# Kernel tuning notes

Hardware: AMD Instinct MI355X
Metric: run time of the kernel (lower is better)

The kernel has to match this reference:

```python
import jax, jax.numpy as jnp
import numpy as np

B, L, D, H, K = 4, 2048, 256, 8, 32
DH = D // H
DE = 64          # d_edge
CLIP = 32        # relpos_clip


def _ln(x, g, b):
    mu = x.mean(-1, keepdims=True)
    var = ((x - mu) ** 2).mean(-1, keepdims=True)
    return (x - mu) / jnp.sqrt(var + 1e-5) * g + b


def _gelu(x):
    return jax.nn.gelu(x, approximate=False)  # torch nn.GELU default = exact erf


def _masked_softmax(logits, mask):
    logits = jnp.where(mask == 0, jnp.finfo(logits.dtype).min, logits)
    return jax.nn.softmax(logits, axis=-1)


def setup_inputs() -> dict:
    key = jax.random.key(0)
    ks = jax.random.split(key, 24)
    s = 0.02
    w = lambda i, shape: jax.random.normal(ks[i], shape, jnp.float32) * s
    p = {}
    p['x'] = jax.random.normal(ks[0], (B, L, D), jnp.float32)
    p['mask'] = jax.random.randint(ks[1], (B, L), 0, 2, jnp.int32)
    p['nbr_idx'] = jax.random.randint(ks[2], (B, L, K), 0, L, jnp.int32)
    p['nbr_mask'] = jax.random.randint(ks[3], (B, L, K), 0, 2, jnp.int32)
    p['rel_pos'] = jax.random.randint(ks[4], (B, L, K), 0, 2 * CLIP + 1, jnp.int32)
    p['g1'] = jnp.ones((D,)); p['b1'] = jnp.zeros((D,))
    p['wq'] = w(5, (D, D)); p['wk'] = w(6, (D, D)); p['wv'] = w(7, (D, D))
    p['relpos_emb'] = w(8, (2 * CLIP + 1, DE))
    p['we1'] = w(9, (DE, D)); p['be1'] = jnp.zeros((D,))
    p['we2'] = w(10, (D, 1)); p['be2'] = jnp.zeros((1,))
    p['wg1'] = w(11, (2 * D, D)); p['bg1'] = jnp.zeros((D,))
    p['wg2'] = w(12, (D, D)); p['bg2'] = jnp.zeros((D,))
    p['wlo'] = w(13, (D, D)); p['blo'] = jnp.zeros((D,))
    p['wqkv'] = w(14, (D, 3 * D)); p['wgo'] = w(15, (D, D))
    p['wf1'] = w(16, (D, D)); p['bf1'] = jnp.zeros((D,))
    p['wf2'] = w(17, (D, 2)); p['bf2'] = jnp.zeros((2,))
    p['g2'] = jnp.ones((D,)); p['b2'] = jnp.zeros((D,))
    p['wff1'] = w(18, (D, 4 * D)); p['bff1'] = jnp.zeros((4 * D,))
    p['wff2'] = w(19, (4 * D, D)); p['bff2'] = jnp.zeros((D,))
    return p


def _block(x, mask, nbr_idx, nbr_mask, rel_pos,
           g1, b1, wq, wk, wv, relpos_emb, we1, be1, we2, be2,
           wg1, bg1, wg2, bg2, wlo, blo, wqkv, wgo,
           wf1, bf1, wf2, bf2, g2, b2, wff1, bff1, wff2, bff2):
    mf = mask.astype(x.dtype)                       # [B,L]
    h = _ln(x, g1, b1)

    # ---- local graph attention (gather over K neighbors) ----
    neigh = jax.vmap(lambda hb, ib: hb[ib])(h, nbr_idx)     # [B,L,K,D]
    q = (h @ wq)[:, :, None, :]                             # [B,L,1,D]
    k = neigh @ wk                                          # [B,L,K,D]
    v = neigh @ wv
    attn = (q * k).sum(-1) / np.sqrt(D).astype(np.float32)  # [B,L,K]
    rel = jnp.clip(rel_pos, -CLIP, CLIP) + CLIP
    e = relpos_emb[rel]                                     # [B,L,K,DE]
    attn = attn + (_gelu(e @ we1 + be1) @ we2 + be2)[..., 0]
    amask = nbr_mask * mask[:, :, None]
    w = _masked_softmax(attn, amask)
    agg = jnp.einsum('blk,blkd->bld', w, v)
    agg = agg @ wlo + blo
    g = jax.nn.sigmoid(_gelu(jnp.concatenate([h, agg], -1) @ wg1 + bg1) @ wg2 + bg2)
    h_local = (h + g * agg) * mf[..., None]

    # ---- global linear attention ----
    qkv = h @ wqkv
    qg, kg, vg = jnp.split(qkv, 3, axis=-1)
    to_heads = lambda z: z.reshape(B, L, H, DH).transpose(0, 2, 1, 3)  # [B,H,L,DH]
    qg, kg, vg = to_heads(qg), to_heads(kg), to_heads(vg)
    phi = lambda z: jax.nn.elu(z) + 1.0
    qg, kg = phi(qg), phi(kg)
    m = mf[:, None, :, None]
    kg = kg * m
    vg = vg * m
    kv = jnp.einsum('bhld,bhlm->bhdm', kg, vg)
    z = 1.0 / (jnp.einsum('bhld,bhd->bhl', qg, kg.sum(axis=2)) + 1e-6)
    y = jnp.einsum('bhld,bhdm->bhlm', qg, kv) * z[..., None]
    y = y.transpose(0, 2, 1, 3).reshape(B, L, D)
    y = (y @ wgo) * mf[..., None]
    h_global = h + y

    # ---- gated fusion (softmax over 2 branches) ----
    fw = jax.nn.softmax(_gelu(h @ wf1 + bf1) @ wf2 + bf2, axis=-1)
    yc = fw[..., 0:1] * h_local + fw[..., 1:2] * h_global
    x2 = x + (yc - x)  # DropPath is identity in eval mode

    # ---- FFN ----
    hn = _ln(x2, g2, b2)
    ffn = _gelu(hn @ wff1 + bff1) @ wff2 + bff2
    out = (x2 + ffn) * mf[..., None]
    return out


def reference(x, mask, nbr_idx, nbr_mask, rel_pos,
              g1, b1, wq, wk, wv, relpos_emb, we1, be1, we2, be2,
              wg1, bg1, wg2, bg2, wlo, blo, wqkv, wgo,
              wf1, bf1, wf2, bf2, g2, b2, wff1, bff1, wff2, bff2):
    return _block(x, mask, nbr_idx, nbr_mask, rel_pos,
                  g1, b1, wq, wk, wv, relpos_emb, we1, be1, we2, be2,
                  wg1, bg1, wg2, bg2, wlo, blo, wqkv, wgo,
                  wf1, bf1, wf2, bf2, g2, b2, wff1, bff1, wff2, bff2)
```

## Files before the change

kernel.cpp:

```cpp
#include <hip/hip_runtime.h>
#include <math.h>

#define LSEQ 2048
#define BB 4
#define DD 256
#define NROWS (BB*LSEQ)
#define LDBIG 1792

typedef unsigned short u16;
typedef unsigned int u32;
typedef short s16x8 __attribute__((ext_vector_type(8)));
typedef float f32x4 __attribute__((ext_vector_type(4)));

#define WT_BIG  0
#define WT_LO   458752
#define WT_G1   524288
#define WT_G2   655360
#define WT_GO   720896
#define WT_FF1  786432
#define WT_FF2  1048576
#define WT_TMP1 1310720
#define WT_TMP2 1376256

__device__ __forceinline__ float gelu_f(float x){
    return 0.5f*x*(1.0f+erff(x*0.70710678118654752440f));
}
__device__ __forceinline__ float phi_f(float z){ return z>0.f ? z+1.f : expf(z); }
__device__ __forceinline__ float bf2f(u16 u){ union{u32 i; float f;} x; x.i = ((u32)u)<<16; return x.f; }
__device__ __forceinline__ u16 f2bf(float f){ union{float f; u32 i;} x; x.f = f; u32 r = (x.i + 0x7fff + ((x.i>>16)&1)) >> 16; return (u16)r; }

struct TransDesc { const float* src; int dstoff; int srcK; int N; int dstStride; int tstart; };
struct TransArgs { TransDesc d[12]; };

__global__ __launch_bounds__(256) void prep_kernel(
    TransArgs args, u16* __restrict__ WT,
    const float* __restrict__ x, const float* __restrict__ g1,
    const float* __restrict__ b1, u16* __restrict__ h,
    const float* __restrict__ emb, const float* __restrict__ we1,
    const float* __restrict__ be1, const float* __restrict__ we2,
    const float* __restrict__ be2, float* __restrict__ btab,
    float* __restrict__ kvz,
    const float* __restrict__ wlo, const float* __restrict__ wg1,
    const float* __restrict__ blo, const float* __restrict__ bg1,
    float* __restrict__ bprime)
{
    int bid = blockIdx.x;
    if (bid < 1280){
        int z = 0;
        #pragma unroll
        for (int i=1;i<12;++i) if (bid >= args.d[i].tstart) z = i;
        TransDesc e = args.d[z];
        int tid = bid - e.tstart;
        int ntx = e.N >> 5;
        int kt = tid / ntx, nt = tid - kt*ntx;
        __shared__ float tile[32][33];
        int tx = threadIdx.x & 31, ty = threadIdx.x >> 5;
        #pragma unroll
        for (int i=0;i<4;++i){
            int k = kt*32 + ty + i*8;
            tile[ty+i*8][tx] = e.src[(size_t)k*e.N + nt*32 + tx];
        }
        __syncthreads();
        #pragma unroll
        for (int i=0;i<4;++i){
            int n = nt*32 + ty + i*8;
            WT[e.dstoff + (size_t)n*e.dstStride + kt*32 + tx] = f2bf(tile[tx][ty+i*8]);
        }
    } else if (bid < 9472){
        int r = bid - 1280; int t = threadIdx.x;
        size_t i = (size_t)r*DD + t;
        float v = x[i];
        float s = v, ss = v*v;
        #pragma unroll
        for (int o=32;o>=1;o>>=1){ s += __shfl_xor(s,o); ss += __shfl_xor(ss,o); }
        __shared__ float sh[8];
        int wave = t>>6, lane = t&63;
        if (lane==0){ sh[wave]=s; sh[4+wave]=ss; }
        __syncthreads();
        float S  = sh[0]+sh[1]+sh[2]+sh[3];
        float SS = sh[4]+sh[5]+sh[6]+sh[7];
        float mu  = S*(1.f/DD);
        float var = SS*(1.f/DD) - mu*mu;
        float inv = rsqrtf(var + 1e-5f);
        h[i] = f2bf((v-mu)*inv*g1[t] + b1[t]);
    } else if (bid < 9537){
        int r = bid - 9472; int j = threadIdx.x;
        float acc = be1[j];
        #pragma unroll 8
        for (int d=0; d<64; ++d) acc += emb[r*64+d]*we1[d*256+j];
        float tv = gelu_f(acc)*we2[j];
        #pragma unroll
        for (int o=32;o>=1;o>>=1) tv += __shfl_xor(tv,o);
        __shared__ float sh2[4];
        int wave = j>>6, lane = j&63;
        if (lane==0) sh2[wave]=tv;
        __syncthreads();
        if (j==0) btab[r] = sh2[0]+sh2[1]+sh2[2]+sh2[3] + be2[0];
    } else if (bid < 9669){
        int idx = (bid - 9537)*256 + threadIdx.x;
        kvz[idx] = 0.f;
    } else if (bid < 9733){
        int idx = (bid - 9669)*1024 + threadIdx.x*4;
        float4 v = *(const float4*)&wlo[idx];
        u32 lo = (u32)f2bf(v.x) | ((u32)f2bf(v.y)<<16);
        u32 hi = (u32)f2bf(v.z) | ((u32)f2bf(v.w)<<16);
        *(u32*)&WT[WT_TMP2 + idx]     = lo;
        *(u32*)&WT[WT_TMP2 + idx + 2] = hi;
    } else {
        int t = threadIdx.x;
        float a = bg1[t];
        for (int m=0;m<256;++m) a += blo[m]*wg1[(size_t)(256+m)*256 + t];
        bprime[t] = a;
    }
}

template<int ACT, bool FINAL, typename CT>
__device__ __forceinline__ void mgemm_core(
    const u16* __restrict__ A0, const u16* __restrict__ A1, int kswitch, int lda,
    const u16* __restrict__ WT, int Kd,
    const float* __restrict__ bias, int actcol,
    CT* __restrict__ C, int ldc,
    const u16* __restrict__ addsrc, const int* __restrict__ rowmask,
    int row0, int col0)
{
    __shared__ u16 ldsA[4096];
    __shared__ u16 ldsB[8192];
    int t = threadIdx.x;
    int l = t & 63, w = t >> 6;
    int wm = w >> 1, wn = w & 1;

    int s_ar = t >> 2, s_ao = t & 3;
    int aidx1 = (s_ar>>4)*1024 + s_ao*128 + (s_ar&15)*8;
    int aidx2 = aidx1 + 4*128;
    int s_bc = t >> 1, s_bo = (t & 1)*4;
    int bbase = (s_bc>>4)*1024 + (s_bc&15)*8;

    f32x4 acc[2][4];
    #pragma unroll
    for (int mf=0;mf<2;++mf)
        #pragma unroll
        for (int nf=0;nf<4;++nf)
            acc[mf][nf] = (f32x4){0.f,0.f,0.f,0.f};

    uint4 av1, av2, bv0, bv1, bv2, bv3;
    {
        const u16* ap = A0 + (size_t)(row0+s_ar)*lda;
        av1 = *(const uint4*)(ap + s_ao*8);
        av2 = *(const uint4*)(ap + 32 + s_ao*8);
        const u16* bp = WT + (size_t)(col0 + s_bc)*Kd + s_bo*8;
        bv0 = *(const uint4*)(bp); bv1 = *(const uint4*)(bp+8);
        bv2 = *(const uint4*)(bp+16); bv3 = *(const uint4*)(bp+24);
    }

    for (int k0 = 0; k0 < Kd; k0 += 64){
        __syncthreads();
        *(uint4*)&ldsA[aidx1] = av1;
        *(uint4*)&ldsA[aidx2] = av2;
        *(uint4*)&ldsB[bbase + (s_bo  )*128] = bv0;
        *(uint4*)&ldsB[bbase + (s_bo+1)*128] = bv1;
        *(uint4*)&ldsB[bbase + (s_bo+2)*128] = bv2;
        *(uint4*)&ldsB[bbase + (s_bo+3)*128] = bv3;
        __syncthreads();
        int kn = k0 + 64;
        if (kn < Kd){
            const u16* Ab = A0; int kk = kn;
            if (kn >= kswitch){ Ab = A1; kk = kn - kswitch; }
            const u16* ap = Ab + (size_t)(row0+s_ar)*lda + kk;
            av1 = *(const uint4*)(ap + s_ao*8);
            av2 = *(const uint4*)(ap + 32 + s_ao*8);
            const u16* bp = WT + (size_t)(col0 + s_bc)*Kd + kn + s_bo*8;
            bv0 = *(const uint4*)(bp); bv1 = *(const uint4*)(bp+8);
            bv2 = *(const uint4*)(bp+16); bv3 = *(const uint4*)(bp+24);
        }
        #pragma unroll
        for (int s=0;s<2;++s){
            s16x8 af[2], bfr[4];
            #pragma unroll
            for (int mf=0;mf<2;++mf) af[mf] = *(s16x8*)&ldsA[(wm*2+mf)*1024 + (s*4+(l>>4))*128 + (l&15)*8];
            #pragma unroll
            for (int nf=0;nf<4;++nf) bfr[nf] = *(s16x8*)&ldsB[(wn*4+nf)*1024 + (s*4+(l>>4))*128 + (l&15)*8];
            #pragma unroll
            for (int mf=0; mf<2; ++mf)
                #pragma unroll
                for (int nf=0; nf<4; ++nf)
                    acc[mf][nf] = __builtin_amdgcn_mfma_f32_16x16x32_bf16(af[mf], bfr[nf], acc[mf][nf], 0,0,0);
        }
    }

    int lrow = (l>>4)*4, lcol = l&15;
    #pragma unroll
    for (int mf=0; mf<2; ++mf){
        #pragma unroll
        for (int nf=0; nf<4; ++nf){
            int col = col0 + wn*64 + nf*16 + lcol;
            float bv;
            if (ACT==1) bv = (col >= actcol) ? bias[col-actcol] : 0.f;
            else        bv = bias ? bias[col] : 0.f;
            #pragma unroll
            for (int i=0;i<4;++i){
                int row = row0 + wm*32 + mf*16 + lrow + i;
                float v = acc[mf][nf][i] + bv;
                if (ACT==1){ if (col >= actcol) v = gelu_f(v); }
                else if (ACT==2) v = 1.f/(1.f+expf(-v));
                if (FINAL){
                    float mfv = (float)rowmask[row];
                    v = (bf2f(addsrc[(size_t)row*ldc + col]) + v) * mfv;
                }
                if constexpr (sizeof(CT)==2) C[(size_t)row*ldc+col] = (CT)f2bf(v);
                else                         C[(size_t)row*ldc+col] = v;
            }
        }
    }
}

template<int ACT, bool FINAL, typename CT>
__global__ __launch_bounds__(256) void mgemm(
    const u16* __restrict__ A0, const u16* __restrict__ A1, int kswitch, int lda,
    const u16* __restrict__ WT, int Kd,
    const float* __restrict__ bias, int actcol,
    CT* __restrict__ C, int ldc,
    const u16* __restrict__ addsrc, const int* __restrict__ rowmask)
{
    mgemm_core<ACT,FINAL,CT>(A0,A1,kswitch,lda,WT,Kd,bias,actcol,C,ldc,addsrc,rowmask,
                             blockIdx.x*64, blockIdx.y*128);
}

struct GemmCfg { const u16* A0; const u16* A1; int kswitch; const u16* WT; int Kd;
                 const float* bias; int act; u16* C; };
__global__ __launch_bounds__(256) void mgemm_tri(GemmCfg c0, GemmCfg c1, GemmCfg c2)
{
    GemmCfg c = (blockIdx.z==0) ? c0 : ((blockIdx.z==1) ? c1 : c2);
    if (c.act==1)
        mgemm_core<1,false,u16>(c.A0, c.A1, c.kswitch, 256, c.WT, c.Kd, c.bias, 0,
                                c.C, 256, nullptr, nullptr, blockIdx.x*64, blockIdx.y*128);
    else
        mgemm_core<0,false,u16>(c.A0, c.A1, c.kswitch, 256, c.WT, c.Kd, c.bias, 0,
                                c.C, 256, nullptr, nullptr, blockIdx.x*64, blockIdx.y*128);
}

__global__ __launch_bounds__(256) void nattn_kernel(
    const u16* __restrict__ nb,
    const int* __restrict__ nbr_idx, const int* __restrict__ nbr_mask,
    const int* __restrict__ rel_pos, const int* __restrict__ mask,
    const float* __restrict__ btab, u16* __restrict__ agg)
{
    int r = blockIdx.x;
    int b = r >> 11;
    int t = threadIdx.x, lane = t&63, wave = t>>6;
    __shared__ float s_w[32];
    __shared__ float s_agg[4][256];
    uint2 qu = *(const uint2*)&nb[(size_t)r*LDBIG + lane*4];
    float q0 = bf2f(qu.x&0xffff), q1 = bf2f(qu.x>>16);
    float q2 = bf2f(qu.y&0xffff), q3 = bf2f(qu.y>>16);
    int mrow = mask[r];

    uint2 kreg[8], vreg[8];
    #pragma unroll
    for (int j=0;j<8;++j){
        int idx = nbr_idx[r*32 + wave*8 + j];
        size_t grow = ((size_t)(b<<11) + idx)*LDBIG;
        kreg[j] = *(const uint2*)&nb[grow + 256 + lane*4];
        vreg[j] = *(const uint2*)&nb[grow + 512 + lane*4];
    }
    float d[8];
    #pragma unroll
    for (int j=0;j<8;++j){
        d[j] = q0*bf2f(kreg[j].x&0xffff) + q1*bf2f(kreg[j].x>>16)
             + q2*bf2f(kreg[j].y&0xffff) + q3*bf2f(kreg[j].y>>16);
    }
    #define CMB(a,b,s) ({ float _t = (lane&(s)) ? (a) : (b); float _r = __shfl_xor(_t,(s)); (lane&(s)) ? ((b)+_r) : ((a)+_r); })
    float e10 = CMB(d[0],d[1],1), e11 = CMB(d[2],d[3],1);
    float e12 = CMB(d[4],d[5],1), e13 = CMB(d[6],d[7],1);
    float e20 = CMB(e10,e11,2),   e21 = CMB(e12,e13,2);
    float e3  = CMB(e20,e21,4);
    #undef CMB
    e3 += __shfl_xor(e3,8); e3 += __shfl_xor(e3,16); e3 += __shfl_xor(e3,32);
    if (lane < 8){
        int k = wave*8 + lane;
        int rp = rel_pos[r*32+k];
        rp = rp < -32 ? -32 : (rp > 32 ? 32 : rp);
        float logit = e3*0.0625f + btab[rp+32];
        int am = nbr_mask[r*32+k] * mrow;
        s_w[k] = am ? logit : -3.402823466e38f;
    }
    __syncthreads();
    if (wave==0){
        float lg = (lane<32) ? s_w[lane] : -3.402823466e38f;
        float m = lg;
        #pragma unroll
        for (int o=16;o>=1;o>>=1) m = fmaxf(m, __shfl_xor(m,o));
        float e = (lane<32) ? expf(lg-m) : 0.f;
        float ssum = e;
        #pragma unroll
        for (int o=16;o>=1;o>>=1) ssum += __shfl_xor(ssum,o);
        if (lane<32) s_w[lane] = e/ssum;
    }
    __syncthreads();
    float4 av = {0.f,0.f,0.f,0.f};
    #pragma unroll
    for (int j=0;j<8;++j){
        float wk = s_w[wave*8 + j];
        av.x += wk*bf2f(vreg[j].x&0xffff); av.y += wk*bf2f(vreg[j].x>>16);
        av.z += wk*bf2f(vreg[j].y&0xffff); av.w += wk*bf2f(vreg[j].y>>16);
    }
    *(float4*)&s_agg[wave][lane*4] = av;
    __syncthreads();
    float sum = s_agg[0][t]+s_agg[1][t]+s_agg[2][t]+s_agg[3][t];
    agg[(size_t)r*256 + t] = f2bf(sum);
}

__global__ __launch_bounds__(256) void linstats_kernel(
    const u16* __restrict__ qkv, const int* __restrict__ mask,
    float* __restrict__ kv, float* __restrict__ ksum)
{
    int blk = blockIdx.x;
    int bh = blk >> 4, ch = blk & 15;
    int b = bh >> 3, hh = bh & 7;
    int t = threadIdx.x;
    int d = t >> 3, m4 = (t & 7)*4;
    __shared__ float sk[8][32], sv[8][32];
    float a0=0,a1=0,a2=0,a3=0, aks=0;
    int l0 = ch*128;
    int half = t >> 7, tt = t & 127;
    int lr = tt >> 4, e2 = (tt & 15)*2;
    for (int g8=0; g8<16; ++g8){
        int l = l0 + g8*8 + lr;
        size_t base = ((size_t)b*LSEQ + l)*LDBIG + (half ? 1280 : 1024) + hh*32 + e2;
        u32 u = *(const u32*)&qkv[base];
        float mf = (float)mask[b*LSEQ + l];
        float x0 = bf2f((u16)(u & 0xffff));
        float x1 = bf2f((u16)(u >> 16));
        if (half==0){ sk[lr][e2] = phi_f(x0)*mf; sk[lr][e2+1] = phi_f(x1)*mf; }
        else        { sv[lr][e2] = x0*mf;        sv[lr][e2+1] = x1*mf; }
        __syncthreads();
        #pragma unroll
        for (int rr=0;rr<8;++rr){
            float kd = sk[rr][d];
            a0 += kd*sv[rr][m4]; a1 += kd*sv[rr][m4+1];
            a2 += kd*sv[rr][m4+2]; a3 += kd*sv[rr][m4+3];
            if ((t&7)==0) aks += kd;
        }
        __syncthreads();
    }
    size_t kb = (size_t)bh*1024 + d*32 + m4;
    atomicAdd(&kv[kb+0],a0); atomicAdd(&kv[kb+1],a1);
    atomicAdd(&kv[kb+2],a2); atomicAdd(&kv[kb+3],a3);
    if ((t&7)==0) atomicAdd(&ksum[bh*32+d], aks);
}

__global__ __launch_bounds__(256) void linapply_kernel(
    const u16* __restrict__ qkv, const float* __restrict__ kv,
    const float* __restrict__ ksum, u16* __restrict__ y)
{
    int r = blockIdx.x; int b = r >> 11;
    int t = threadIdx.x;
    __shared__ float sq[256];
    if (t < 128){
        u32 u = *(const u32*)&qkv[(size_t)r*LDBIG + 768 + t*2];
        sq[t*2]   = phi_f(bf2f((u16)(u & 0xffff)));
        sq[t*2+1] = phi_f(bf2f((u16)(u >> 16)));
    }
    __syncthreads();
    int hh = t>>5, m = t&31;
    const float* kvb = &kv[(size_t)((b<<3)+hh)*1024 + m];
    const float* ksb = &ksum[((b<<3)+hh)*32];
    const float* sqh = &sq[hh*32];
    float acc=0.f, az=0.f;
    #pragma unroll
    for (int dd=0; dd<32; ++dd){
        float qd = sqh[dd];
        acc += qd * kvb[dd*32];
        az  += qd * ksb[dd];
    }
    y[(size_t)r*256 + t] = f2bf(acc / (az + 1e-6f));
}

__global__ __launch_bounds__(128) void combine_kernel(
    const u16* __restrict__ h, const u16* __restrict__ agglo,
    const u16* __restrict__ g, const u16* __restrict__ ygo,
    const u16* __restrict__ bigout, const float* __restrict__ wf2,
    const float* __restrict__ bf2v, const int* __restrict__ mask,
    const float* __restrict__ g2, const float* __restrict__ b2,
    u16* __restrict__ x2, u16* __restrict__ hn)
{
    int r = blockIdx.x, t = threadIdx.x;
    int wave = t>>6, lane = t&63;
    u32 fu = *(const u32*)&bigout[(size_t)r*LDBIG + 1536 + t*2];
    float fa = bf2f((u16)(fu&0xffff)), fb = bf2f((u16)(fu>>16));
    int dd = t*2;
    float p0 = fa*wf2[dd*2]   + fb*wf2[dd*2+2];
    float p1 = fa*wf2[dd*2+1] + fb*wf2[dd*2+3];
    #pragma unroll
    for (int o=32;o>=1;o>>=1){ p0 += __shfl_xor(p0,o); p1 += __shfl_xor(p1,o); }
    __shared__ float shp[4];
    if (lane==0){ shp[wave]=p0; shp[2+wave]=p1; }
    __syncthreads();
    float P0 = shp[0]+shp[1]+bf2v[0], P1 = shp[2]+shp[3]+bf2v[1];
    float mx = fmaxf(P0,P1);
    float e0 = expf(P0-mx), e1 = expf(P1-mx);
    float f0 = e0/(e0+e1), f1v = e1/(e0+e1);
    size_t i = (size_t)r*DD + t*2;
    float mf = (float)mask[r];
    u32 hu = *(const u32*)&h[i],  au = *(const u32*)&agglo[i];
    u32 gu = *(const u32*)&g[i],  yu = *(const u32*)&ygo[i];
    float hv0 = bf2f((u16)(hu&0xffff)), hv1 = bf2f((u16)(hu>>16));
    float ag0 = bf2f((u16)(au&0xffff)), ag1 = bf2f((u16)(au>>16));
    float gg0 = bf2f((u16)(gu&0xffff)), gg1 = bf2f((u16)(gu>>16));
    float yy0 = bf2f((u16)(yu&0xffff)), yy1 = bf2f((u16)(yu>>16));
    float v0 = f0*((hv0 + gg0*ag0)*mf) + f1v*(hv0 + yy0*mf);
    float v1 = f0*((hv1 + gg1*ag1)*mf) + f1v*(hv1 + yy1*mf);
    *(u32*)&x2[i] = (u32)f2bf(v0) | ((u32)f2bf(v1)<<16);
    float s = v0+v1, ss = v0*v0+v1*v1;
    #pragma unroll
    for (int o=32;o>=1;o>>=1){ s += __shfl_xor(s,o); ss += __shfl_xor(ss,o); }
    __shared__ float sh[4];
    if (lane==0){ sh[wave]=s; sh[2+wave]=ss; }
    __syncthreads();
    float S  = sh[0]+sh[1];
    float SS = sh[2]+sh[3];
    float mu  = S*(1.f/DD);
    float var = SS*(1.f/DD) - mu*mu;
    float inv = rsqrtf(var + 1e-5f);
    int j0 = t*2;
    float o0 = (v0-mu)*inv*g2[j0]   + b2[j0];
    float o1 = (v1-mu)*inv*g2[j0+1] + b2[j0+1];
    *(u32*)&hn[i] = (u32)f2bf(o0) | ((u32)f2bf(o1)<<16);
}

extern "C" void kernel_launch(void* const* d_in, const int* in_sizes, int n_in,
                              void* d_out, int out_size, void* d_ws, size_t ws_size,
                              hipStream_t stream)
{
    const float* x        = (const float*)d_in[0];
    const int*   mask     = (const int*)  d_in[1];
    const int*   nbr_idx  = (const int*)  d_in[2];
    const int*   nbr_mask = (const int*)  d_in[3];
    const int*   rel_pos  = (const int*)  d_in[4];
    const float* g1   = (const float*)d_in[5];
    const float* b1   = (const float*)d_in[6];
    const float* wq   = (const float*)d_in[7];
    const float* wk   = (const float*)d_in[8];
    const float* wv   = (const float*)d_in[9];
    const float* relpos_emb = (const float*)d_in[10];
    const float* we1  = (const float*)d_in[11];
    const float* be1  = (const float*)d_in[12];
    const float* we2  = (const float*)d_in[13];
    const float* be2  = (const float*)d_in[14];
    const float* wg1  = (const float*)d_in[15];
    const float* bg1  = (const float*)d_in[16];
    const float* wg2  = (const float*)d_in[17];
    const float* bg2  = (const float*)d_in[18];
    const float* wlo  = (const float*)d_in[19];
    const float* blo  = (const float*)d_in[20];
    const float* wqkv = (const float*)d_in[21];
    const float* wgo  = (const float*)d_in[22];
    const float* wf1  = (const float*)d_in[23];
    const float* bf1  = (const float*)d_in[24];
    const float* wf2  = (const float*)d_in[25];
    const float* bf2  = (const float*)d_in[26];
    const float* g2   = (const float*)d_in[27];
    const float* b2   = (const float*)d_in[28];
    const float* wff1 = (const float*)d_in[29];
    const float* bff1 = (const float*)d_in[30];
    const float* wff2 = (const float*)d_in[31];
    const float* bff2 = (const float*)d_in[32];
    float* out = (float*)d_out;

    unsigned char* wsb = (unsigned char*)d_ws;
    u16* bigout  = (u16*)(wsb + ((size_t)0<<20));
    u16* h_bf    = (u16*)(wsb + ((size_t)30<<20));
    u16* agg_bf  = (u16*)(wsb + ((size_t)34<<20));
    u16* agglo_bf= (u16*)(wsb + ((size_t)38<<20));
    u16* x2y_bf  = (u16*)(wsb + ((size_t)42<<20));
    u16* tg_bf   = (u16*)(wsb + ((size_t)46<<20));
    u16* ygo_bf  = (u16*)(wsb + ((size_t)50<<20));
    u16* hn_bf   = (u16*)(wsb + ((size_t)54<<20));
    u16* WT      = (u16*)(wsb + ((size_t)58<<20));
    float* btab  = (float*)(wsb + ((size_t)61<<20));
    float* kvb   = btab + 128;
    float* ksb   = kvb + 32768;
    float* bprime= ksb + 1024;

    TransArgs ta;
    ta.d[0]  = { wq,          WT_BIG + 0,       256,  256,  256,    0 };
    ta.d[1]  = { wk,          WT_BIG + 65536,   256,  256,  256,   64 };
    ta.d[2]  = { wv,          WT_BIG + 131072,  256,  256,  256,  128 };
    ta.d[3]  = { wqkv,        WT_BIG + 196608,  256,  768,  256,  192 };
    ta.d[4]  = { wf1,         WT_BIG + 393216,  256,  256,  256,  384 };
    ta.d[5]  = { wlo,         WT_LO,            256,  256,  256,  448 };
    ta.d[6]  = { wg1,         WT_G1,            256,  256,  512,  512 };
    ta.d[7]  = { wg2,         WT_G2,            256,  256,  256,  576 };
    ta.d[8]  = { wgo,         WT_GO,            256,  256,  256,  640 };
    ta.d[9]  = { wff1,        WT_FF1,           256, 1024,  256,  704 };
    ta.d[10] = { wff2,        WT_FF2,          1024,  256, 1024,  960 };
    ta.d[11] = { wg1+65536,   WT_TMP1,          256,  256,  256, 1216 };

    const int KBIG = 1<<30;
    dim3 blk(256);

    prep_kernel<<<9734, blk, 0, stream>>>(ta, WT, x, g1, b1, h_bf,
                                          relpos_emb, we1, be1, we2, be2, btab, kvb,
                                          wlo, wg1, blo, bg1, bprime);
    mgemm<0,false,u16><<<dim3(4,2), blk, 0, stream>>>(WT+WT_TMP1, WT+WT_TMP1, KBIG, 256,
                                                      WT+WT_TMP2, 256, nullptr, 0,
                                                      WT+WT_G1+256, 512, nullptr, nullptr);
    mgemm<1,false,u16><<<dim3(128,14), blk, 0, stream>>>(h_bf, h_bf, KBIG, 256, WT+WT_BIG, 256, bf1, 1536, bigout, LDBIG, nullptr, nullptr);
    linstats_kernel<<<512, blk, 0, stream>>>(bigout, mask, kvb, ksb);
    linapply_kernel<<<NROWS, blk, 0, stream>>>(bigout, kvb, ksb, x2y_bf);
    nattn_kernel<<<NROWS, blk, 0, stream>>>(bigout, nbr_idx, nbr_mask, rel_pos, mask, btab, agg_bf);
    {
        GemmCfg cgo = { x2y_bf, x2y_bf, KBIG, WT+WT_GO, 256, nullptr, 0, ygo_bf };
        GemmCfg clo = { agg_bf, agg_bf, KBIG, WT+WT_LO, 256, blo,     0, agglo_bf };
        GemmCfg cg1 = { h_bf,   agg_bf, 256,  WT+WT_G1, 512, bprime,  1, tg_bf };
        mgemm_tri<<<dim3(128,2,3), blk, 0, stream>>>(cgo, clo, cg1);
    }
    mgemm<2,false,u16><<<dim3(128,2), blk, 0, stream>>>(tg_bf, tg_bf, KBIG, 256, WT+WT_G2, 256, bg2, 0, agg_bf, 256, nullptr, nullptr);
    combine_kernel<<<NROWS, dim3(128), 0, stream>>>(h_bf, agglo_bf, agg_bf, ygo_bf, bigout, wf2, bf2, mask, g2, b2, x2y_bf, hn_bf);
    mgemm<1,false,u16><<<dim3(128,8), blk, 0, stream>>>(hn_bf, hn_bf, KBIG, 256, WT+WT_FF1, 256, bff1, 0, bigout, 1024, nullptr, nullptr);
    mgemm<0,true,float><<<dim3(128,2), blk, 0, stream>>>(bigout, bigout, KBIG, 1024, WT+WT_FF2, 1024, bff2, 0, out, 256, x2y_bf, mask);
}
```

Measured before the change: 285.2 us.

## Fuse gate GEMM with fusion/LayerNorm combine; shuffle-based softmax in neighbor attention

The separate wg2 GEMM (sigmoid gate) and the per-row combine kernel are merged into one kernel. Each block computes a 32-row by 256-column gate tile with MFMA, then applies the branch-softmax fusion, writes x2 and computes LayerNorm for hn in the same kernel. This removes one launch and the round-trip of the gate tensor through global memory. In exchange, only 256 blocks are launched, which may underuse the GPU, and the epilogue uses scattered 2-byte stores. The neighbor-attention softmax now runs redundantly in every wave with shuffles, replacing a wave-0-only pass plus an extra barrier.

After: 293.7 us. +3.0%, slower.

```diff
diff --git a/kernel.cpp b/kernel.cpp
--- a/kernel.cpp
+++ b/kernel.cpp
@@ -284,22 +284,19 @@
         s_w[k] = am ? logit : -3.402823466e38f;
     }
     __syncthreads();
-    if (wave==0){
-        float lg = (lane<32) ? s_w[lane] : -3.402823466e38f;
-        float m = lg;
-        #pragma unroll
-        for (int o=16;o>=1;o>>=1) m = fmaxf(m, __shfl_xor(m,o));
-        float e = (lane<32) ? expf(lg-m) : 0.f;
-        float ssum = e;
-        #pragma unroll
-        for (int o=16;o>=1;o>>=1) ssum += __shfl_xor(ssum,o);
-        if (lane<32) s_w[lane] = e/ssum;
-    }
-    __syncthreads();
+    float lg = s_w[lane & 31];
+    float m = lg;
+    #pragma unroll
+    for (int o=16;o>=1;o>>=1) m = fmaxf(m, __shfl_xor(m,o));
+    float e = expf(lg - m);
+    float ssum = e;
+    #pragma unroll
+    for (int o=16;o>=1;o>>=1) ssum += __shfl_xor(ssum,o);
+    float wn = e / ssum;
     float4 av = {0.f,0.f,0.f,0.f};
     #pragma unroll
     for (int j=0;j<8;++j){
-        float wk = s_w[wave*8 + j];
+        float wk = __shfl(wn, wave*8 + j);
         av.x += wk*bf2f(vreg[j].x&0xffff); av.y += wk*bf2f(vreg[j].x>>16);
         av.z += wk*bf2f(vreg[j].y&0xffff); av.w += wk*bf2f(vreg[j].y>>16);
     }
@@ -375,56 +372,165 @@
     y[(size_t)r*256 + t] = f2bf(acc / (az + 1e-6f));
 }
 
-__global__ __launch_bounds__(128) void combine_kernel(
+__global__ __launch_bounds__(256) void gcombine_kernel(
+    const u16* __restrict__ tg, const u16* __restrict__ WTg2,
+    const float* __restrict__ bg2,
     const u16* __restrict__ h, const u16* __restrict__ agglo,
-    const u16* __restrict__ g, const u16* __restrict__ ygo,
-    const u16* __restrict__ bigout, const float* __restrict__ wf2,
-    const float* __restrict__ bf2v, const int* __restrict__ mask,
-    const float* __restrict__ g2, const float* __restrict__ b2,
+    const u16* __restrict__ ygo, const u16* __restrict__ bigout,
+    const float* __restrict__ wf2, const float* __restrict__ bf2v,
+    const int* __restrict__ mask, const float* __restrict__ g2,
+    const float* __restrict__ b2,
     u16* __restrict__ x2, u16* __restrict__ hn)
 {
-    int r = blockIdx.x, t = threadIdx.x;
-    int wave = t>>6, lane = t&63;
-    u32 fu = *(const u32*)&bigout[(size_t)r*LDBIG + 1536 + t*2];
-    float fa = bf2f((u16)(fu&0xffff)), fb = bf2f((u16)(fu>>16));
-    int dd = t*2;
-    float p0 = fa*wf2[dd*2]   + fb*wf2[dd*2+2];
-    float p1 = fa*wf2[dd*2+1] + fb*wf2[dd*2+3];
-    #pragma unroll
-    for (int o=32;o>=1;o>>=1){ p0 += __shfl_xor(p0,o); p1 += __shfl_xor(p1,o); }
-    __shared__ float shp[4];
-    if (lane==0){ shp[wave]=p0; shp[2+wave]=p1; }
+    __shared__ u16 ldsA[2048];
+    __shared__ u16 ldsB[16384];
+    __shared__ float s_fw0[32], s_fw1[32];
+    __shared__ float s_rs[4][32], s_rss[4][32];
+    int t = threadIdx.x;
+    int row0 = blockIdx.x*32;
+    int l = t & 63, w = t >> 6;
+
+    {
+        int rl = t>>3, seg = t&7;
+        const u16* f1p = bigout + (size_t)(row0+rl)*LDBIG + 1536 + seg*32;
+        float p0=0.f, p1=0.f;
+        #pragma unroll
+        for (int c=0;c<32;c+=2){
+            u32 u = *(const u32*)&f1p[c];
+            float a = bf2f((u16)(u&0xffff)), bb = bf2f((u16)(u>>16));
+            int col = seg*32+c;
+            p0 += a*wf2[col*2]   + bb*wf2[col*2+2];
+            p1 += a*wf2[col*2+1] + bb*wf2[col*2+3];
+        }
+        p0 += __shfl_xor(p0,1); p1 += __shfl_xor(p1,1);
+        p0 += __shfl_xor(p0,2); p1 += __shfl_xor(p1,2);
+        p0 += __shfl_xor(p0,4); p1 += __shfl_xor(p1,4);
+        if ((t&7)==0){
+            float P0 = p0 + bf2v[0], P1 = p1 + bf2v[1];
+            float mx = fmaxf(P0,P1);
+            float e0 = expf(P0-mx), e1 = expf(P1-mx);
+            float si = 1.f/(e0+e1);
+            s_fw0[rl] = e0*si; s_fw1[rl] = e1*si;
+        }
+    }
+
+    int s_ar = t >> 2, s_ao = t & 3;
+    int aidx1 = (s_ar>>4)*1024 + s_ao*128 + (s_ar&15)*8;
+    int aidx2 = aidx1 + 512;
+    int bidx = (t>>4)*1024 + (t&15)*8;
+
+    f32x4 acc[2][4];
+    #pragma unroll
+    for (int mf=0;mf<2;++mf)
+        #pragma unroll
+        for (int nf=0;nf<4;++nf)
+            acc[mf][nf] = (f32x4){0.f,0.f,0.f,0.f};
+
+    uint4 av1, av2, bv[8];
+    {
+        if (t < 128){
+            const u16* ap = tg + (size_t)(row0+s_ar)*256;
+            av1 = *(const uint4*)(ap + s_ao*8);
+            av2 = *(const uint4*)(ap + 32 + s_ao*8);
+        }
+        const u16* bp = WTg2 + (size_t)t*256;
+        #pragma unroll
+        for (int o=0;o<8;++o) bv[o] = *(const uint4*)(bp + o*8);
+    }
+
+    for (int k0 = 0; k0 < 256; k0 += 64){
+        __syncthreads();
+        if (t < 128){
+            *(uint4*)&ldsA[aidx1] = av1;
+            *(uint4*)&ldsA[aidx2] = av2;
+        }
+        #pragma unroll
+        for (int o=0;o<8;++o) *(uint4*)&ldsB[bidx + o*128] = bv[o];
+        __syncthreads();
+        int kn = k0 + 64;
+        if (kn < 256){
+            if (t < 128){
+                const u16* ap = tg + (size_t)(row0+s_ar)*256 + kn;
+                av1 = *(const uint4*)(ap + s_ao*8);
+                av2 = *(const uint4*)(ap + 32 + s_ao*8);
+            }
+            const u16* bp = WTg2 + (size_t)t*256 + kn;
+            #pragma unroll
+            for (int o=0;o<8;++o) bv[o] = *(const uint4*)(bp + o*8);
+        }
+        #pragma unroll
+        for (int s=0;s<2;++s){
+            s16x8 af[2], bfr[4];
+            #pragma unroll
+            for (int mf=0;mf<2;++mf) af[mf] = *(s16x8*)&ldsA[mf*1024 + (s*4+(l>>4))*128 + (l&15)*8];
+            #pragma unroll
+            for (int nf=0;nf<4;++nf) bfr[nf] = *(s16x8*)&ldsB[(w*4+nf)*1024 + (s*4+(l>>4))*128 + (l&15)*8];
+            #pragma unroll
+            for (int mf=0; mf<2; ++mf)
+                #pragma unroll
+                for (int nf=0; nf<4; ++nf)
+                    acc[mf][nf] = __builtin_amdgcn_mfma_f32_16x16x32_bf16(af[mf], bfr[nf], acc[mf][nf], 0,0,0);
+        }
+    }
+
+    int lrow = (l>>4)*4, lcol = l&15;
+    float vbuf[2][4][4];
+    #pragma unroll
+    for (int mf=0; mf<2; ++mf){
+        #pragma unroll
+        for (int nf=0; nf<4; ++nf){
+            int col = w*64 + nf*16 + lcol;
+            float bvv = bg2[col];
+            #pragma unroll
+            for (int i=0;i<4;++i){
+                int rloc = mf*16 + lrow + i;
+                int row = row0 + rloc;
+                float gv = 1.f/(1.f+expf(-(acc[mf][nf][i] + bvv)));
+                float mfv = (float)mask[row];
+                size_t idx = (size_t)row*256 + col;
+                float hv = bf2f(h[idx]), ag = bf2f(agglo[idx]), yy = bf2f(ygo[idx]);
+                float f0 = s_fw0[rloc], f1v = s_fw1[rloc];
+                float v = f0*((hv + gv*ag)*mfv) + f1v*(hv + yy*mfv);
+                x2[idx] = f2bf(v);
+                vbuf[mf][nf][i] = v;
+            }
+        }
+    }
+    #pragma unroll
+    for (int mf=0; mf<2; ++mf){
+        #pragma unroll
+        for (int i=0;i<4;++i){
+            float s = vbuf[mf][0][i]+vbuf[mf][1][i]+vbuf[mf][2][i]+vbuf[mf][3][i];
+            float ss = vbuf[mf][0][i]*vbuf[mf][0][i]+vbuf[mf][1][i]*vbuf[mf][1][i]
+                     + vbuf[mf][2][i]*vbuf[mf][2][i]+vbuf[mf][3][i]*vbuf[mf][3][i];
+            #pragma unroll
+            for (int o=8;o>=1;o>>=1){ s += __shfl_xor(s,o); ss += __shfl_xor(ss,o); }
+            if (lcol==0){
+                int rloc = mf*16 + lrow + i;
+                s_rs[w][rloc] = s; s_rss[w][rloc] = ss;
+            }
+        }
+    }
     __syncthreads();
-    float P0 = shp[0]+shp[1]+bf2v[0], P1 = shp[2]+shp[3]+bf2v[1];
-    float mx = fmaxf(P0,P1);
-    float e0 = expf(P0-mx), e1 = expf(P1-mx);
-    float f0 = e0/(e0+e1), f1v = e1/(e0+e1);
-    size_t i = (size_t)r*DD + t*2;
-    float mf = (float)mask[r];
-    u32 hu = *(const u32*)&h[i],  au = *(const u32*)&agglo[i];
-    u32 gu = *(const u32*)&g[i],  yu = *(const u32*)&ygo[i];
-    float hv0 = bf2f((u16)(hu&0xffff)), hv1 = bf2f((u16)(hu>>16));
-    float ag0 = bf2f((u16)(au&0xffff)), ag1 = bf2f((u16)(au>>16));
-    float gg0 = bf2f((u16)(gu&0xffff)), gg1 = bf2f((u16)(gu>>16));
-    float yy0 = bf2f((u16)(yu&0xffff)), yy1 = bf2f((u16)(yu>>16));
-    float v0 = f0*((hv0 + gg0*ag0)*mf) + f1v*(hv0 + yy0*mf);
-    float v1 = f0*((hv1 + gg1*ag1)*mf) + f1v*(hv1 + yy1*mf);
-    *(u32*)&x2[i] = (u32)f2bf(v0) | ((u32)f2bf(v1)<<16);
-    float s = v0+v1, ss = v0*v0+v1*v1;
-    #pragma unroll
-    for (int o=32;o>=1;o>>=1){ s += __shfl_xor(s,o); ss += __shfl_xor(ss,o); }
-    __shared__ float sh[4];
-    if (lane==0){ sh[wave]=s; sh[2+wave]=ss; }
-    __syncthreads();
-    float S  = sh[0]+sh[1];
-    float SS = sh[2]+sh[3];
-    float mu  = S*(1.f/DD);
-    float var = SS*(1.f/DD) - mu*mu;
-    float inv = rsqrtf(var + 1e-5f);
-    int j0 = t*2;
-    float o0 = (v0-mu)*inv*g2[j0]   + b2[j0];
-    float o1 = (v1-mu)*inv*g2[j0+1] + b2[j0+1];
-    *(u32*)&hn[i] = (u32)f2bf(o0) | ((u32)f2bf(o1)<<16);
+    #pragma unroll
+    for (int mf=0; mf<2; ++mf){
+        #pragma unroll
+        for (int i=0;i<4;++i){
+            int rloc = mf*16 + lrow + i;
+            float S  = s_rs[0][rloc]+s_rs[1][rloc]+s_rs[2][rloc]+s_rs[3][rloc];
+            float SS = s_rss[0][rloc]+s_rss[1][rloc]+s_rss[2][rloc]+s_rss[3][rloc];
+            float mu  = S*(1.f/DD);
+            float var = SS*(1.f/DD) - mu*mu;
+            float inv = rsqrtf(var + 1e-5f);
+            int row = row0 + rloc;
+            #pragma unroll
+            for (int nf=0;nf<4;++nf){
+                int col = w*64 + nf*16 + lcol;
+                float o = (vbuf[mf][nf][i]-mu)*inv*g2[col] + b2[col];
+                hn[(size_t)row*256 + col] = f2bf(o);
+            }
+        }
+    }
 }
 
 extern "C" void kernel_launch(void* const* d_in, const int* in_sizes, int n_in,
@@ -514,8 +620,9 @@
         GemmCfg cg1 = { h_bf,   agg_bf, 256,  WT+WT_G1, 512, bprime,  1, tg_bf };
         mgemm_tri<<<dim3(128,2,3), blk, 0, stream>>>(cgo, clo, cg1);
     }
-    mgemm<2,false,u16><<<dim3(128,2), blk, 0, stream>>>(tg_bf, tg_bf, KBIG, 256, WT+WT_G2, 256, bg2, 0, agg_bf, 256, nullptr, nullptr);
-    combine_kernel<<<NROWS, dim3(128), 0, stream>>>(h_bf, agglo_bf, agg_bf, ygo_bf, bigout, wf2, bf2, mask, g2, b2, x2y_bf, hn_bf);
+    gcombine_kernel<<<256, blk, 0, stream>>>(tg_bf, WT+WT_G2, bg2,
+                                             h_bf, agglo_bf, ygo_bf, bigout,
+                                             wf2, bf2, mask, g2, b2, x2y_bf, hn_bf);
     mgemm<1,false,u16><<<dim3(128,8), blk, 0, stream>>>(hn_bf, hn_bf, KBIG, 256, WT+WT_FF1, 256, bff1, 0, bigout, 1024, nullptr, nullptr);
     mgemm<0,true,float><<<dim3(128,2), blk, 0, stream>>>(bigout, bigout, KBIG, 1024, WT+WT_FF2, 1024, bff2, 0, out, 256, x2y_bf, mask);
 }
```
